# Performance work log

Measured on AMD Instinct MI355X. Metric: run time of the kernel, lower is better.

## Reference

```python
import jax, jax.numpy as jnp
import numpy as np
from jax import lax

T, C_IN, H, W = 15, 6, 160, 160
F1, K1, THR1 = 30, 5, 15.0
F2, K2, THR2 = 250, 3, 10.0
KWTA2, RADIUS2 = 8, 1


def conv2d(x, w):
    # x: [T, Cin, H, W] (time occupies the batch slot, SpykeTorch style); w: [Cout, Cin, k, k]
    return lax.conv_general_dilated(x, w, (1, 1), 'VALID',
                                    dimension_numbers=('NCHW', 'OIHW', 'NCHW'))


def fire(pot, thr):
    # torch.nn.functional.threshold_(pot, thr, 0): keep strictly-greater values
    p = jnp.where(pot > thr, pot, 0.0)
    return jnp.sign(p), p


def max_pool(x, k, s):
    return lax.reduce_window(x, -jnp.inf, lax.max, (1, 1, k, k), (1, 1, s, s), 'VALID')


def pad_hw(x, p):
    return jnp.pad(x, ((0, 0), (0, 0), (p, p), (p, p)))


def pointwise_inhibition(pot):
    # pot: [T, F, H, W] thresholded potentials (cumulative spike encoding over T).
    # At each spatial position keep only the feature that spiked earliest (via the
    # per-timestep max feature at the first spiking timestep); zero all others.
    t = pot.shape[0]
    max_val = pot.max(axis=1, keepdims=True)      # [T,1,H,W]
    max_idx = pot.argmax(axis=1, keepdims=True)   # [T,1,H,W]
    clamp = jnp.sign(max_val)                     # spike indicator of per-position max
    first_t = jnp.clip((t - clamp.sum(axis=0, keepdims=True)).astype(jnp.int32), 0, t - 1)
    last = clamp[-1:]                             # [1,1,H,W]: 1 if position ever spiked
    winner_f = jnp.take_along_axis(max_idx, first_t, axis=0)  # [1,1,H,W]
    f_range = jnp.arange(pot.shape[1]).reshape(1, -1, 1, 1)
    coef = jnp.where(f_range == winner_f, last, 0.0)          # scatter_(1, winners, last)
    return pot * coef


def get_k_winners(pot, spikes, kwta, radius):
    # Faithful jit-friendly version of sf.get_k_winners: rank by (spiked-early, potential),
    # iteratively pick the max, suppress its whole feature map and a (2r+1)^2 spatial
    # window across all features (NMS-like).
    t, f, h, w = pot.shape
    first_t = jnp.clip((t - spikes.sum(axis=0)).astype(jnp.int32), 0, t - 1)  # [F,H,W]
    values = jnp.take_along_axis(pot, first_t[None], axis=0)[0]  # earliest potential per neuron
    truncated = spikes * values[None]
    v = truncated.max() * t
    total = (truncated + spikes * v).sum(axis=0)  # [F,H,W]
    hs, ws = jnp.arange(h), jnp.arange(w)

    def step(tot, _):
        idx = jnp.argmax(tot)
        val = tot.reshape(-1)[idx]
        valid = val != 0.0
        fi = idx // (h * w)
        hi = (idx % (h * w)) // w
        wi = idx % w
        tot = jnp.where(valid, tot.at[fi].set(0.0), tot)  # block the winning feature
        sp = (jnp.abs(hs - hi)[:, None] <= radius) & (jnp.abs(ws - wi)[None, :] <= radius)
        tot = jnp.where(valid & sp[None], 0.0, tot)       # columnar spatial inhibition
        win = jnp.where(valid, jnp.stack([fi, hi, wi]), -1)
        return tot, win

    _, winners = lax.scan(step, total, None, length=kwta)
    return winners  # [kwta, 3] (feature, row, col), -1 rows = no winner


def setup_inputs():
    key = jax.random.key(0)
    k1, k2, k3 = jax.random.split(key, 3)
    # Cumulative spike-wave input: each (c,h,w) neuron fires at most once; spikes accumulate over T.
    u = jax.random.uniform(k1, (T, C_IN, H, W), dtype=jnp.float32)
    data = jnp.clip(jnp.cumsum((u < 0.05).astype(jnp.float32), axis=0), 0.0, 1.0)
    W1 = 0.8 + 0.05 * jax.random.normal(k2, (F1, C_IN, K1, K1), dtype=jnp.float32)
    W2 = 0.8 + 0.05 * jax.random.normal(k3, (F2, F1, K2, K2), dtype=jnp.float32)
    return {"data": data, "W1": W1, "W2": W2}


def reference(data, W1, W2):
    x = pad_hw(data, 2)                                  # sf.pad(data, (2,2,2,2))
    spike1, _ = fire(conv2d(x, W1), THR1)                # conv1 + fire(thr=15)
    inp2 = pad_hw(max_pool(spike1, 2, 2), 1)             # pool(2,2) + pad(1,1,1,1)
    _, pot2 = fire(conv2d(inp2, W2), THR2)               # conv2 + fire(thr=10)
    pot2 = pointwise_inhibition(pot2)                    # lateral inhibition
    spike2 = jnp.sign(pot2)
    winners = get_k_winners(pot2, spike2, KWTA2, RADIUS2)  # k=8, r=1 spatial k-WTA
    return spike2, pot2, winners
```

## Files before the change

### kernel.cpp

```cpp
#include <hip/hip_runtime.h>
#include <cstdint>

#define T_    15
#define C1    6
#define F1    30
#define THR1  15.0f
#define F2    250
#define THR2  10.0f
#define WP    80
#define NLOC  6400
#define KWTA  8
#define P1R   164
#define P1S   (164*164)
#define P2R   84
#define P2S   (84*84)
#define POT_OFF 24000000
#define WIN_OFF 48000000

typedef unsigned long long u64;

__global__ void k_pad(const float* __restrict__ data, float* __restrict__ P1) {
    int idx = blockIdx.x * 256 + threadIdx.x;
    int x = idx % 160;
    int y = (idx / 160) % 160;
    int tc = idx / 25600;
    P1[(size_t)tc * P1S + (size_t)(y + 2) * P1R + (x + 2)] = data[idx];
}

__global__ __launch_bounds__(256) void k_conv1(const float* __restrict__ P1,
                                               const float* __restrict__ W1,
                                               float* __restrict__ P2) {
    int lane = threadIdx.x & 63;
    int wv   = __builtin_amdgcn_readfirstlane(threadIdx.x >> 6);
    int f    = blockIdx.y * 4 + wv;
    int fw   = f < F1 ? f : F1 - 1;
    int ty   = blockIdx.x / 5, tx = blockIdx.x % 5;
    int t    = blockIdx.z;
    int py   = lane >> 2, pxg = lane & 3;
    int rowb = 32 * ty + 2 * py;
    int cb   = 32 * tx + 8 * pxg;
    const float* p1 = P1 + (size_t)(t * C1) * P1S;

    float a0[8], a1[8];
    #pragma unroll
    for (int i = 0; i < 8; i++) { a0[i] = 0.f; a1[i] = 0.f; }

    for (int c = 0; c < C1; c++) {
        const float* pc = p1 + (size_t)c * P1S;
        const float* wc = W1 + (fw * C1 + c) * 25;
        #pragma unroll
        for (int r = 0; r < 6; r++) {
            const float4* rp = (const float4*)(pc + (size_t)(rowb + r) * P1R + cb);
            float4 u0 = rp[0], u1 = rp[1], u2 = rp[2];
            float d[12] = {u0.x,u0.y,u0.z,u0.w, u1.x,u1.y,u1.z,u1.w, u2.x,u2.y,u2.z,u2.w};
            if (r <= 4) {
                #pragma unroll
                for (int kx = 0; kx < 5; kx++) {
                    float w = wc[r * 5 + kx];
                    #pragma unroll
                    for (int cc = 0; cc < 8; cc++) a0[cc] += w * d[cc + kx];
                }
            }
            if (r >= 1) {
                #pragma unroll
                for (int kx = 0; kx < 5; kx++) {
                    float w = wc[(r - 1) * 5 + kx];
                    #pragma unroll
                    for (int cc = 0; cc < 8; cc++) a1[cc] += w * d[cc + kx];
                }
            }
        }
    }
    if (f < F1) {
        float* p2 = P2 + (size_t)(t * F1 + f) * P2S;
        int prow = 1 + 16 * ty + py;
        int pcol = 1 + 16 * tx + 4 * pxg;
        #pragma unroll
        for (int q = 0; q < 4; q++) {
            bool s = (a0[2*q] > THR1) || (a0[2*q+1] > THR1) ||
                     (a1[2*q] > THR1) || (a1[2*q+1] > THR1);
            p2[(size_t)prow * P2R + pcol + q] = s ? 1.0f : 0.0f;
        }
    }
}

__global__ void k_wprep(const float* __restrict__ W2, float* __restrict__ W2T) {
    int f   = threadIdx.x;
    int blk = blockIdx.x;
    W2T[blk * 256 + f] = (f < F2) ? W2[f * 270 + blk] : 0.f;
}

__global__ __launch_bounds__(256) void k_conv2max(const float* __restrict__ P2,
                                                  const float* __restrict__ W2T,
                                                  float* __restrict__ pot,
                                                  u64* __restrict__ gkey) {
    __shared__ u64 skey[4 * 256];
    int lane = threadIdx.x & 63;
    int wv   = __builtin_amdgcn_readfirstlane(threadIdx.x >> 6);
    int f0   = blockIdx.y * 32 + wv * 8;
    int ty   = blockIdx.x / 5, tx = blockIdx.x % 5;
    int t    = blockIdx.z;
    int py   = lane >> 2, pxg = lane & 3;
    int row  = 16 * ty + py;
    int cx   = 16 * tx + 4 * pxg;
    const float* pin = P2 + (size_t)(t * F1) * P2S;

    float acc[8][4];
    #pragma unroll
    for (int j = 0; j < 8; j++)
        #pragma unroll
        for (int q = 0; q < 4; q++) acc[j][q] = 0.f;

    for (int c = 0; c < F1; c++) {
        const float* pc = pin + (size_t)c * P2S;
        const float* wb = W2T + (size_t)(c * 9) * 256 + f0;
        #pragma unroll
        for (int ky = 0; ky < 3; ky++) {
            const float4* rp = (const float4*)(pc + (size_t)(row + ky) * P2R + cx);
            float4 u0 = rp[0], u1 = rp[1];
            float d[8] = {u0.x,u0.y,u0.z,u0.w, u1.x,u1.y,u1.z,u1.w};
            #pragma unroll
            for (int kx = 0; kx < 3; kx++) {
                const float* wp = wb + (ky * 3 + kx) * 256;
                #pragma unroll
                for (int j = 0; j < 8; j++) {
                    float w = wp[j];
                    acc[j][0] += w * d[kx + 0];
                    acc[j][1] += w * d[kx + 1];
                    acc[j][2] += w * d[kx + 2];
                    acc[j][3] += w * d[kx + 3];
                }
            }
        }
    }

    u64 best[4] = {0, 0, 0, 0};
    #pragma unroll
    for (int j = 0; j < 8; j++) {
        int f = f0 + j;
        float4 r;
        r.x = acc[j][0] > THR2 ? acc[j][0] : 0.f;
        r.y = acc[j][1] > THR2 ? acc[j][1] : 0.f;
        r.z = acc[j][2] > THR2 ? acc[j][2] : 0.f;
        r.w = acc[j][3] > THR2 ? acc[j][3] : 0.f;
        if (f < F2)
            *(float4*)(pot + ((size_t)t * F2 + f) * NLOC + (size_t)row * WP + cx) = r;
        u64 lo = (u64)(unsigned)(255 - f);
        u64 k0 = ((u64)__float_as_uint(r.x) << 32) | lo;
        u64 k1 = ((u64)__float_as_uint(r.y) << 32) | lo;
        u64 k2 = ((u64)__float_as_uint(r.z) << 32) | lo;
        u64 k3 = ((u64)__float_as_uint(r.w) << 32) | lo;
        best[0] = best[0] > k0 ? best[0] : k0;
        best[1] = best[1] > k1 ? best[1] : k1;
        best[2] = best[2] > k2 ? best[2] : k2;
        best[3] = best[3] > k3 ? best[3] : k3;
    }
    int sb = py * 16 + pxg * 4;
    #pragma unroll
    for (int q = 0; q < 4; q++) skey[wv * 256 + sb + q] = best[q];
    __syncthreads();
    int tid = threadIdx.x;
    u64 k0 = skey[tid], k1 = skey[256 + tid], k2 = skey[512 + tid], k3 = skey[768 + tid];
    u64 ka = k0 > k1 ? k0 : k1;
    u64 kb = k2 > k3 ? k2 : k3;
    u64 kk = ka > kb ? ka : kb;
    int r = tid >> 4, cc = tid & 15;
    gkey[(size_t)(blockIdx.y * T_ + t) * NLOC + (size_t)(16 * ty + r) * WP + 16 * tx + cc] = kk;
}

__global__ void k_red(const u64* __restrict__ gkey, const float* __restrict__ pot,
                      int* __restrict__ winf, int* __restrict__ nsA,
                      float* __restrict__ vfA, float* __restrict__ colv,
                      unsigned* __restrict__ vmax) {
    int loc = blockIdx.x * 256 + threadIdx.x;
    float mv[T_]; int mi[T_];
    #pragma unroll
    for (int t = 0; t < T_; t++) {
        u64 best = 0;
        #pragma unroll
        for (int g = 0; g < 8; g++) {
            u64 k = gkey[(size_t)(g * T_ + t) * NLOC + loc];
            best = best > k ? best : k;
        }
        mv[t] = __uint_as_float((unsigned)(best >> 32));
        mi[t] = 255 - (int)(best & 0xFFFFFFFFu);
    }
    int nclamp = 0;
    #pragma unroll
    for (int t = 0; t < T_; t++) nclamp += (mv[t] > 0.f);
    int ft = T_ - nclamp; if (ft > T_ - 1) ft = T_ - 1;
    int winner = -1;
    #pragma unroll
    for (int t = 0; t < T_; t++) if (t == ft) winner = mi[t];
    bool last = mv[T_ - 1] > 0.f;
    if (!last) winner = -1;
    winf[loc] = winner;

    float col[T_];
    #pragma unroll
    for (int t = 0; t < T_; t++) col[t] = 0.f;
    if (winner >= 0) {
        const float* p = pot + (size_t)winner * NLOC + loc;
        #pragma unroll
        for (int t = 0; t < T_; t++) col[t] = p[(size_t)t * F2 * NLOC];
    }
    int ns = 0;
    #pragma unroll
    for (int t = 0; t < T_; t++) ns += (col[t] > 0.f);
    int f2 = T_ - ns; if (f2 > T_ - 1) f2 = T_ - 1;
    float vf = 0.f;
    #pragma unroll
    for (int t = 0; t < T_; t++) if (t == f2) vf = col[t];
    nsA[loc] = ns; vfA[loc] = vf;
    #pragma unroll
    for (int t = 0; t < T_; t++) colv[t * NLOC + loc] = col[t];
    atomicMax(vmax, __float_as_uint(vf));
}

__global__ void k_zero(float* __restrict__ outbuf, const int* __restrict__ winf,
                       const float* __restrict__ colv) {
    int idx = blockIdx.x * 256 + threadIdx.x;
    if (idx >= T_ * F2 * (NLOC / 4)) return;
    int l4 = idx % (NLOC / 4);
    int f  = (idx / (NLOC / 4)) % F2;
    int t  = idx / ((NLOC / 4) * F2);
    int loc = l4 * 4;
    int4   wf = *(const int4*)(winf + loc);
    float4 cv = *(const float4*)(colv + t * NLOC + loc);
    float4 po, sp;
    po.x = (wf.x == f) ? cv.x : 0.f;  sp.x = po.x > 0.f ? 1.f : 0.f;
    po.y = (wf.y == f) ? cv.y : 0.f;  sp.y = po.y > 0.f ? 1.f : 0.f;
    po.z = (wf.z == f) ? cv.z : 0.f;  sp.z = po.z > 0.f ? 1.f : 0.f;
    po.w = (wf.w == f) ? cv.w : 0.f;  sp.w = po.w > 0.f ? 1.f : 0.f;
    size_t off = ((size_t)t * F2 + f) * NLOC + loc;
    *(float4*)(outbuf + POT_OFF + off) = po;
    *(float4*)(outbuf + off) = sp;
}

__global__ __launch_bounds__(256) void k_winners(const int* __restrict__ winf,
                                                 const int* __restrict__ nsA,
                                                 const float* __restrict__ vfA,
                                                 const unsigned* __restrict__ vmax,
                                                 float* __restrict__ wout) {
    __shared__ float tot[NLOC];
    __shared__ int   wfl[NLOC];
    __shared__ float rv[256];
    __shared__ int   rk[256];
    __shared__ float bvS; __shared__ int fiS, hiS, wiS;
    int tid = threadIdx.x;
    float v = __uint_as_float(vmax[0]) * (float)T_;
    for (int l = tid; l < NLOC; l += 256) {
        tot[l] = (float)nsA[l] * (vfA[l] + v);
        wfl[l] = winf[l];
    }
    __syncthreads();
    for (int it = 0; it < KWTA; it++) {
        float bv = 0.f; int bk = 0x7fffffff;
        #pragma unroll
        for (int i = 0; i < 25; i++) {
            int l = tid * 25 + i;
            float vv = tot[l];
            int k = wfl[l] * NLOC + l;
            if (vv > bv || (vv == bv && k < bk)) { bv = vv; bk = k; }
        }
        rv[tid] = bv; rk[tid] = bk;
        __syncthreads();
        for (int s = 128; s > 0; s >>= 1) {
            if (tid < s) {
                float v2 = rv[tid + s]; int k2 = rk[tid + s];
                if (v2 > rv[tid] || (v2 == rv[tid] && k2 < rk[tid])) { rv[tid] = v2; rk[tid] = k2; }
            }
            __syncthreads();
        }
        if (tid == 0) {
            float bvv = rv[0]; int bkk = rk[0];
            bool valid = bvv > 0.f;
            int fi = valid ? bkk / NLOC : -1;
            int lc = bkk % NLOC;
            int hi = valid ? lc / WP : -1;
            int wi = valid ? lc % WP : -1;
            wout[it * 3 + 0] = (float)fi;
            wout[it * 3 + 1] = (float)hi;
            wout[it * 3 + 2] = (float)wi;
            bvS = bvv; fiS = fi; hiS = hi; wiS = wi;
        }
        __syncthreads();
        if (bvS > 0.f) {
            #pragma unroll
            for (int i = 0; i < 25; i++) {
                int l = tid * 25 + i;
                int h = l / WP, w = l % WP;
                bool kill = (wfl[l] == fiS) ||
                            (h >= hiS - 1 && h <= hiS + 1 && w >= wiS - 1 && w <= wiS + 1);
                if (kill) tot[l] = 0.f;
            }
        }
        __syncthreads();
    }
}

extern "C" void kernel_launch(void* const* d_in, const int* in_sizes, int n_in,
                              void* d_out, int out_size, void* d_ws, size_t ws_size,
                              hipStream_t stream) {
    const float* data = (const float*)d_in[0];
    const float* W1   = (const float*)d_in[1];
    const float* W2   = (const float*)d_in[2];
    float* out = (float*)d_out;
    float* ws  = (float*)d_ws;

    float*    P1   = ws;
    float*    P2   = ws + 2420640;
    float*    W2T  = ws + 5595840;
    int*      winf = (int*)(ws + 5664960);
    int*      nsA  = (int*)(ws + 5671360);
    float*    vfA  = ws + 5677760;
    float*    colv = ws + 5684160;
    unsigned* vmax = (unsigned*)(ws + 5780160);

    u64* gkey = (u64*)d_out;
    float* potD = out + POT_OFF;

    hipMemsetAsync(P1, 0, 2420640 * sizeof(float), stream);
    hipMemsetAsync(P2, 0, 3175200 * sizeof(float), stream);
    hipMemsetAsync(vmax, 0, sizeof(unsigned), stream);

    k_pad     <<<9000, 256, 0, stream>>>(data, P1);
    k_conv1   <<<dim3(25, 8, T_), 256, 0, stream>>>(P1, W1, P2);
    k_wprep   <<<270, 256, 0, stream>>>(W2, W2T);
    k_conv2max<<<dim3(25, 8, T_), 256, 0, stream>>>(P2, W2T, potD, gkey);
    k_red     <<<25, 256, 0, stream>>>(gkey, potD, winf, nsA, vfA, colv, vmax);
    k_zero    <<<(T_ * F2 * (NLOC / 4) + 255) / 256, 256, 0, stream>>>(out, winf, colv);
    k_winners <<<1, 256, 0, stream>>>(winf, nsA, vfA, vmax, out + WIN_OFF);
}
```

Baseline: 455.8 us.

## Run conv2 argmax on bf16 MFMA and recompute only winner potentials

Conv2 moves from scalar FP32 FMAs to bf16 MFMA 16x16x32 instructions. Weights are split into high/mid/low bf16 parts to approximate FP32 precision, and the input spikes (0/1) are exact in bf16. The full 250-feature potential tensor is no longer written. Only a per-location max key is produced, and a new kernel recomputes the winner feature's potential exactly in FP32 for each timestep. This removes a large global write and the scalar conv cost, but the argmax now rests on an approximate split-bf16 sum, so near ties could pick a different feature.

```diff
diff --git a/kernel.cpp b/kernel.cpp
--- a/kernel.cpp
+++ b/kernel.cpp
@@ -18,6 +18,17 @@
 #define WIN_OFF 48000000
 
 typedef unsigned long long u64;
+typedef unsigned short u16;
+typedef short s16x8 __attribute__((ext_vector_type(8)));
+typedef float f32x4 __attribute__((ext_vector_type(4)));
+
+static __device__ __forceinline__ u16 f2bf(float x) {
+    unsigned u = __float_as_uint(x);
+    return (u16)((u + 0x7FFF + ((u >> 16) & 1)) >> 16);
+}
+static __device__ __forceinline__ float bf2f(u16 h) {
+    return __uint_as_float(((unsigned)h) << 16);
+}
 
 __global__ void k_pad(const float* __restrict__ data, float* __restrict__ P1) {
     int idx = blockIdx.x * 256 + threadIdx.x;
@@ -84,126 +95,150 @@
     }
 }
 
-__global__ void k_wprep(const float* __restrict__ W2, float* __restrict__ W2T) {
-    int f   = threadIdx.x;
-    int blk = blockIdx.x;
-    W2T[blk * 256 + f] = (f < F2) ? W2[f * 270 + blk] : 0.f;
-}
-
-__global__ __launch_bounds__(256) void k_conv2max(const float* __restrict__ P2,
-                                                  const float* __restrict__ W2T,
-                                                  float* __restrict__ pot,
-                                                  u64* __restrict__ gkey) {
-    __shared__ u64 skey[4 * 256];
-    int lane = threadIdx.x & 63;
-    int wv   = __builtin_amdgcn_readfirstlane(threadIdx.x >> 6);
-    int f0   = blockIdx.y * 32 + wv * 8;
-    int ty   = blockIdx.x / 5, tx = blockIdx.x % 5;
-    int t    = blockIdx.z;
-    int py   = lane >> 2, pxg = lane & 3;
-    int row  = 16 * ty + py;
-    int cx   = 16 * tx + 4 * pxg;
-    const float* pin = P2 + (size_t)(t * F1) * P2S;
-
-    float acc[8][4];
-    #pragma unroll
-    for (int j = 0; j < 8; j++)
-        #pragma unroll
-        for (int q = 0; q < 4; q++) acc[j][q] = 0.f;
-
-    for (int c = 0; c < F1; c++) {
-        const float* pc = pin + (size_t)c * P2S;
-        const float* wb = W2T + (size_t)(c * 9) * 256 + f0;
-        #pragma unroll
-        for (int ky = 0; ky < 3; ky++) {
-            const float4* rp = (const float4*)(pc + (size_t)(row + ky) * P2R + cx);
-            float4 u0 = rp[0], u1 = rp[1];
-            float d[8] = {u0.x,u0.y,u0.z,u0.w, u1.x,u1.y,u1.z,u1.w};
-            #pragma unroll
-            for (int kx = 0; kx < 3; kx++) {
-                const float* wp = wb + (ky * 3 + kx) * 256;
+__global__ void k_wprep(const float* __restrict__ W2, u16* __restrict__ Wf) {
+    int E = blockIdx.x * 256 + threadIdx.x;
+    int j    = E & 7;
+    int lane = (E >> 3) & 63;
+    int ft   = (E >> 9) & 15;
+    int rest = E >> 13;
+    int s = rest / 9, g = rest % 9;
+    int c = (lane >> 4) * 8 + j;
+    int f = ft * 16 + (lane & 15);
+    float w = (c < F1 && f < F2) ? W2[f * 270 + c * 9 + g] : 0.f;
+    u16 h = f2bf(w);          float fh = bf2f(h);
+    u16 m = f2bf(w - fh);     float fm = bf2f(m);
+    u16 l = f2bf(w - fh - fm);
+    Wf[E] = (s == 0) ? h : (s == 1) ? m : l;
+}
+
+__global__ __launch_bounds__(256) void k_conv2m(const float* __restrict__ P2,
+                                                const u16* __restrict__ Wf,
+                                                u64* __restrict__ gkey) {
+    __shared__ u16 rawT[6 * 18 * 32];
+    __shared__ u64 skey[4 * 4 * 16];
+    int tid  = threadIdx.x;
+    int lane = tid & 63;
+    int wv   = __builtin_amdgcn_readfirstlane(tid >> 6);
+    int bx   = blockIdx.x;
+    int t    = blockIdx.y;
+    int xt = bx % 5, yt = bx / 5;
+    int y0 = yt * 4, x0 = xt * 16;
+
+    for (int e = tid; e < 3456; e += 256) {
+        int c = e / 108, rem = e % 108, r = rem / 18, col = rem % 18;
+        float v = (c < F1)
+            ? P2[(size_t)(t * F1 + c) * P2S + (size_t)(y0 + r) * P2R + (x0 + col)] : 0.f;
+        rawT[(r * 18 + col) * 32 + c] = f2bf(v);
+    }
+    __syncthreads();
+
+    int q = lane >> 4, n = lane & 15;
+    f32x4 accA[4][4], accB[4][4];
+    #pragma unroll
+    for (int j = 0; j < 4; j++)
+        #pragma unroll
+        for (int nt = 0; nt < 4; nt++) { accA[j][nt] = (f32x4)0.f; accB[j][nt] = (f32x4)0.f; }
+
+    #pragma unroll
+    for (int ky = 0; ky < 3; ky++) {
+        #pragma unroll
+        for (int kx = 0; kx < 3; kx++) {
+            int g = ky * 3 + kx;
+            s16x8 bf[4];
+            #pragma unroll
+            for (int nt = 0; nt < 4; nt++)
+                bf[nt] = *(const s16x8*)&rawT[((nt + ky) * 18 + (n + kx)) * 32 + q * 8];
+            #pragma unroll
+            for (int s = 0; s < 3; s++) {
                 #pragma unroll
-                for (int j = 0; j < 8; j++) {
-                    float w = wp[j];
-                    acc[j][0] += w * d[kx + 0];
-                    acc[j][1] += w * d[kx + 1];
-                    acc[j][2] += w * d[kx + 2];
-                    acc[j][3] += w * d[kx + 3];
+                for (int j = 0; j < 4; j++) {
+                    s16x8 af = *(const s16x8*)&Wf[(size_t)((((s * 9 + g) * 16) + (wv * 4 + j)) * 64 + lane) * 8];
+                    f32x4* accp = (s == 0) ? accA[j] : accB[j];
+                    #pragma unroll
+                    for (int nt = 0; nt < 4; nt++)
+                        accp[nt] = __builtin_amdgcn_mfma_f32_16x16x32_bf16(af, bf[nt], accp[nt], 0, 0, 0);
                 }
             }
         }
     }
 
-    u64 best[4] = {0, 0, 0, 0};
-    #pragma unroll
-    for (int j = 0; j < 8; j++) {
-        int f = f0 + j;
-        float4 r;
-        r.x = acc[j][0] > THR2 ? acc[j][0] : 0.f;
-        r.y = acc[j][1] > THR2 ? acc[j][1] : 0.f;
-        r.z = acc[j][2] > THR2 ? acc[j][2] : 0.f;
-        r.w = acc[j][3] > THR2 ? acc[j][3] : 0.f;
-        if (f < F2)
-            *(float4*)(pot + ((size_t)t * F2 + f) * NLOC + (size_t)row * WP + cx) = r;
-        u64 lo = (u64)(unsigned)(255 - f);
-        u64 k0 = ((u64)__float_as_uint(r.x) << 32) | lo;
-        u64 k1 = ((u64)__float_as_uint(r.y) << 32) | lo;
-        u64 k2 = ((u64)__float_as_uint(r.z) << 32) | lo;
-        u64 k3 = ((u64)__float_as_uint(r.w) << 32) | lo;
-        best[0] = best[0] > k0 ? best[0] : k0;
-        best[1] = best[1] > k1 ? best[1] : k1;
-        best[2] = best[2] > k2 ? best[2] : k2;
-        best[3] = best[3] > k3 ? best[3] : k3;
-    }
-    int sb = py * 16 + pxg * 4;
-    #pragma unroll
-    for (int q = 0; q < 4; q++) skey[wv * 256 + sb + q] = best[q];
+    #pragma unroll
+    for (int nt = 0; nt < 4; nt++) {
+        u64 best = 0;
+        #pragma unroll
+        for (int j = 0; j < 4; j++) {
+            #pragma unroll
+            for (int r = 0; r < 4; r++) {
+                float pot = accA[j][nt][r] + accB[j][nt][r];
+                float rr  = pot > THR2 ? pot : 0.f;
+                int f = (wv * 4 + j) * 16 + q * 4 + r;
+                u64 key = ((u64)__float_as_uint(rr) << 32) | (u64)(unsigned)(255 - f);
+                best = best > key ? best : key;
+            }
+        }
+        u64 o = __shfl_xor(best, 16, 64); best = best > o ? best : o;
+        o     = __shfl_xor(best, 32, 64); best = best > o ? best : o;
+        if (q == 0) skey[(wv * 4 + nt) * 16 + n] = best;
+    }
     __syncthreads();
-    int tid = threadIdx.x;
-    u64 k0 = skey[tid], k1 = skey[256 + tid], k2 = skey[512 + tid], k3 = skey[768 + tid];
-    u64 ka = k0 > k1 ? k0 : k1;
-    u64 kb = k2 > k3 ? k2 : k3;
-    u64 kk = ka > kb ? ka : kb;
-    int r = tid >> 4, cc = tid & 15;
-    gkey[(size_t)(blockIdx.y * T_ + t) * NLOC + (size_t)(16 * ty + r) * WP + 16 * tx + cc] = kk;
-}
-
-__global__ void k_red(const u64* __restrict__ gkey, const float* __restrict__ pot,
-                      int* __restrict__ winf, int* __restrict__ nsA,
-                      float* __restrict__ vfA, float* __restrict__ colv,
-                      unsigned* __restrict__ vmax) {
+    if (tid < 64) {
+        int nt2 = tid >> 4, n2 = tid & 15;
+        u64 b = skey[nt2 * 16 + n2];
+        #pragma unroll
+        for (int w = 1; w < 4; w++) {
+            u64 k = skey[(w * 4 + nt2) * 16 + n2];
+            b = b > k ? b : k;
+        }
+        gkey[(size_t)t * NLOC + (size_t)(y0 + nt2) * WP + (x0 + n2)] = b;
+    }
+}
+
+__global__ void k_col(const u64* __restrict__ gkey, const float* __restrict__ P2,
+                      const float* __restrict__ W2, int* __restrict__ winf,
+                      float* __restrict__ colv) {
+    int idx = blockIdx.x * 256 + threadIdx.x;
+    int t   = idx / NLOC;
+    int loc = idx % NLOC;
+    float mv[T_]; int mi[T_];
+    #pragma unroll
+    for (int t2 = 0; t2 < T_; t2++) {
+        u64 k = gkey[(size_t)t2 * NLOC + loc];
+        mv[t2] = __uint_as_float((unsigned)(k >> 32));
+        mi[t2] = 255 - (int)(k & 0xFFFFFFFFu);
+    }
+    int nclamp = 0;
+    #pragma unroll
+    for (int t2 = 0; t2 < T_; t2++) nclamp += (mv[t2] > 0.f);
+    int ft = T_ - nclamp; if (ft > T_ - 1) ft = T_ - 1;
+    int wf = -1;
+    #pragma unroll
+    for (int t2 = 0; t2 < T_; t2++) if (t2 == ft) wf = mi[t2];
+    if (!(mv[T_ - 1] > 0.f)) wf = -1;
+    if (t == 0) winf[loc] = wf;
+
+    float acc = 0.f;
+    if (wf >= 0) {
+        int y = loc / WP, x = loc % WP;
+        const float* pb = P2 + (size_t)(t * F1) * P2S + (size_t)y * P2R + x;
+        const float* wb = W2 + wf * 270;
+        for (int c = 0; c < F1; c++) {
+            #pragma unroll
+            for (int ky = 0; ky < 3; ky++)
+                #pragma unroll
+                for (int kx = 0; kx < 3; kx++)
+                    acc += wb[c * 9 + ky * 3 + kx] * pb[(size_t)c * P2S + ky * P2R + kx];
+    }
+    }
+    acc = acc > THR2 ? acc : 0.f;
+    colv[t * NLOC + loc] = acc;
+}
+
+__global__ void k_stat(const float* __restrict__ colv, int* __restrict__ nsA,
+                       float* __restrict__ vfA, unsigned* __restrict__ vmax) {
     int loc = blockIdx.x * 256 + threadIdx.x;
-    float mv[T_]; int mi[T_];
-    #pragma unroll
-    for (int t = 0; t < T_; t++) {
-        u64 best = 0;
-        #pragma unroll
-        for (int g = 0; g < 8; g++) {
-            u64 k = gkey[(size_t)(g * T_ + t) * NLOC + loc];
-            best = best > k ? best : k;
-        }
-        mv[t] = __uint_as_float((unsigned)(best >> 32));
-        mi[t] = 255 - (int)(best & 0xFFFFFFFFu);
-    }
-    int nclamp = 0;
-    #pragma unroll
-    for (int t = 0; t < T_; t++) nclamp += (mv[t] > 0.f);
-    int ft = T_ - nclamp; if (ft > T_ - 1) ft = T_ - 1;
-    int winner = -1;
-    #pragma unroll
-    for (int t = 0; t < T_; t++) if (t == ft) winner = mi[t];
-    bool last = mv[T_ - 1] > 0.f;
-    if (!last) winner = -1;
-    winf[loc] = winner;
-
     float col[T_];
     #pragma unroll
-    for (int t = 0; t < T_; t++) col[t] = 0.f;
-    if (winner >= 0) {
-        const float* p = pot + (size_t)winner * NLOC + loc;
-        #pragma unroll
-        for (int t = 0; t < T_; t++) col[t] = p[(size_t)t * F2 * NLOC];
-    }
+    for (int t = 0; t < T_; t++) col[t] = colv[t * NLOC + loc];
     int ns = 0;
     #pragma unroll
     for (int t = 0; t < T_; t++) ns += (col[t] > 0.f);
@@ -212,8 +247,6 @@
     #pragma unroll
     for (int t = 0; t < T_; t++) if (t == f2) vf = col[t];
     nsA[loc] = ns; vfA[loc] = vf;
-    #pragma unroll
-    for (int t = 0; t < T_; t++) colv[t * NLOC + loc] = col[t];
     atomicMax(vmax, __float_as_uint(vf));
 }
 
@@ -310,25 +343,25 @@
 
     float*    P1   = ws;
     float*    P2   = ws + 2420640;
-    float*    W2T  = ws + 5595840;
-    int*      winf = (int*)(ws + 5664960);
-    int*      nsA  = (int*)(ws + 5671360);
-    float*    vfA  = ws + 5677760;
-    float*    colv = ws + 5684160;
-    unsigned* vmax = (unsigned*)(ws + 5780160);
+    u16*      Wf   = (u16*)(ws + 5595840);
+    int*      winf = (int*)(ws + 5706432);
+    int*      nsA  = (int*)(ws + 5712832);
+    float*    vfA  = ws + 5719232;
+    float*    colv = ws + 5725632;
+    unsigned* vmax = (unsigned*)(ws + 5821632);
 
     u64* gkey = (u64*)d_out;
-    float* potD = out + POT_OFF;
 
     hipMemsetAsync(P1, 0, 2420640 * sizeof(float), stream);
     hipMemsetAsync(P2, 0, 3175200 * sizeof(float), stream);
     hipMemsetAsync(vmax, 0, sizeof(unsigned), stream);
 
-    k_pad     <<<9000, 256, 0, stream>>>(data, P1);
-    k_conv1   <<<dim3(25, 8, T_), 256, 0, stream>>>(P1, W1, P2);
-    k_wprep   <<<270, 256, 0, stream>>>(W2, W2T);
-    k_conv2max<<<dim3(25, 8, T_), 256, 0, stream>>>(P2, W2T, potD, gkey);
-    k_red     <<<25, 256, 0, stream>>>(gkey, potD, winf, nsA, vfA, colv, vmax);
-    k_zero    <<<(T_ * F2 * (NLOC / 4) + 255) / 256, 256, 0, stream>>>(out, winf, colv);
-    k_winners <<<1, 256, 0, stream>>>(winf, nsA, vfA, vmax, out + WIN_OFF);
-}
+    k_pad    <<<9000, 256, 0, stream>>>(data, P1);
+    k_conv1  <<<dim3(25, 8, T_), 256, 0, stream>>>(P1, W1, P2);
+    k_wprep  <<<864, 256, 0, stream>>>(W2, Wf);
+    k_conv2m <<<dim3(100, T_), 256, 0, stream>>>(P2, Wf, gkey);
+    k_col    <<<375, 256, 0, stream>>>(gkey, P2, W2, winf, colv);
+    k_stat   <<<25, 256, 0, stream>>>(colv, nsA, vfA, vmax);
+    k_zero   <<<(T_ * F2 * (NLOC / 4) + 255) / 256, 256, 0, stream>>>(out, winf, colv);
+    k_winners<<<1, 256, 0, stream>>>(winf, nsA, vfA, vmax, out + WIN_OFF);
+}
```

Measured after the change: 410.1 us. 1.11x faster.
